# Optimization experiments

Hardware: AMD Instinct MI355X
Metric: run time of the kernel (lower is better)

Reference implementation:

```python
import jax, jax.numpy as jnp
import numpy as np

B, N, C, H = 2, 2048, 512, 8
D = C // H  # head dim = 64
SCALE = C ** -0.5  # module uses heads_channels**-0.5 (full inner dim, not per-head)


def setup_inputs() -> dict:
    key = jax.random.key(0)
    ks = jax.random.split(key, 9)
    return {
        "q": jax.random.normal(ks[0], (B, N, C), jnp.float32),
        "kv": jax.random.normal(ks[1], (B, N, C), jnp.float32),
        "pos_q": jax.random.normal(ks[2], (B, N, D), jnp.float32),
        "pos_k": jax.random.normal(ks[3], (B, N, D), jnp.float32),
        "Wq": jax.random.normal(ks[4], (C, C), jnp.float32) * (C ** -0.5),
        "Wk": jax.random.normal(ks[5], (C, C), jnp.float32) * (C ** -0.5),
        "Wv": jax.random.normal(ks[6], (C, C), jnp.float32) * (C ** -0.5),
        "Wo": jax.random.normal(ks[7], (C, C), jnp.float32) * (C ** -0.5),
        "bo": jnp.zeros((C,), jnp.float32),
    }


def reference(q, kv, pos_q, pos_k, Wq, Wk, Wv, Wo, bo):
    # projections: [b n c] @ [c c] -> [b n c]
    qp = q @ Wq
    kp = kv @ Wk
    vp = kv @ Wv
    # split heads: b n (h d) -> b h n d
    split = lambda t: t.reshape(B, N, H, D).transpose(0, 2, 1, 3)
    qh, kh, vh = split(qp), split(kp), split(vp)
    # additive positional bias, broadcast over heads: b n d -> b 1 n d
    qh = qh + pos_q[:, None, :, :]
    kh = kh + pos_k[:, None, :, :]
    sim = jnp.einsum("bhid,bhjd->bhij", qh, kh) * SCALE
    attn = jax.nn.softmax(sim, axis=-1)
    out = jnp.einsum("bhij,bhjd->bhid", attn, vh)
    # merge heads: b h n d -> b n (h d)
    out = out.transpose(0, 2, 1, 3).reshape(B, N, C)
    return out @ Wo + bo
```

## Files before the change

### kernel.cpp

```cpp
#include <hip/hip_runtime.h>
#include <hip/hip_bf16.h>
#include <stdint.h>
#include <math.h>

static constexpr int kB = 2, kN = 2048, kC = 512, kH = 8, kD = 64;
static constexpr float kScaleL2E =
    (float)(0.044194173824159216 * 1.4426950408889634);
static constexpr float kShift = 12.0f;
static constexpr int kSplit = 4;
static constexpr size_t kSegF = (size_t)kB * kN * kC;

typedef short bf16x8 __attribute__((ext_vector_type(8)));
typedef short bf16x4 __attribute__((ext_vector_type(4)));
typedef float f32x4  __attribute__((ext_vector_type(4)));

__device__ __forceinline__ float bf2f(unsigned short u) {
  union { unsigned int i; float f; } v; v.i = ((unsigned int)u) << 16; return v.f;
}
__device__ __forceinline__ unsigned short f2bf(float f) {
  union { float f; unsigned int i; } v; v.f = f;
  unsigned int x = v.i;
  return (unsigned short)((x + 0x7FFFu + ((x >> 16) & 1u)) >> 16);
}
__device__ __forceinline__ short f2bs(float f) { return (short)f2bf(f); }
__device__ __forceinline__ unsigned int pack2_t(float lo, float hi) {
  union { float f; unsigned int i; } a, b; a.f = lo; b.f = hi;
  return (b.i & 0xFFFF0000u) | (a.i >> 16);
}

__device__ __forceinline__ int vcol(int k) {
  return 32 * (k >> 5) + ((k >> 2) & 3) * 8 + ((k >> 4) & 1) * 4;
}

__global__ __launch_bounds__(256) void prep_kernel(
    const float* __restrict__ q, const float* __restrict__ kv,
    const float* __restrict__ Wq, const float* __restrict__ Wk,
    const float* __restrict__ Wv,
    unsigned short* __restrict__ qbf, unsigned short* __restrict__ kvbf,
    unsigned short* __restrict__ wT)
{
  const int t = threadIdx.x;
  if (blockIdx.z == 0) {
    const int gid = blockIdx.x * 256 + t;
    #pragma unroll
    for (int it = 0; it < 8; ++it) {
      int i4 = gid + it * 65536;
      float4 a = *(const float4*)(q + (size_t)i4 * 4);
      float4 b = *(const float4*)(kv + (size_t)i4 * 4);
      bf16x4 ab = {f2bs(a.x), f2bs(a.y), f2bs(a.z), f2bs(a.w)};
      bf16x4 bb = {f2bs(b.x), f2bs(b.y), f2bs(b.z), f2bs(b.w)};
      *(bf16x4*)(qbf + (size_t)i4 * 4) = ab;
      *(bf16x4*)(kvbf + (size_t)i4 * 4) = bb;
    }
  } else {
    if (blockIdx.x >= 192) return;
    const int wsel = blockIdx.x >> 6;
    const int tile = blockIdx.x & 63;
    const int tr = tile >> 3, tc = tile & 7;
    const float* W = (wsel == 0) ? Wq : (wsel == 1 ? Wk : Wv);
    unsigned short* out = wT + (size_t)wsel * kC * kC;

    __shared__ __align__(16) float Ts[64][68];
    #pragma unroll
    for (int it = 0; it < 4; ++it) {
      int e = t + it * 256;
      int r = e >> 4, c4 = (e & 15) * 4;
      *(float4*)&Ts[r][c4] =
          *(const float4*)(W + (size_t)(tr * 64 + r) * kC + tc * 64 + c4);
    }
    __syncthreads();
    const int n = t >> 2, ks = (t & 3) * 16;
    unsigned short* orow = out + (size_t)(tc * 64 + n) * kC + tr * 64 + ks;
    #pragma unroll
    for (int c = 0; c < 4; ++c) {
      ushort4 o;
      o.x = f2bf(Ts[ks + c * 4 + 0][n]);
      o.y = f2bf(Ts[ks + c * 4 + 1][n]);
      o.z = f2bf(Ts[ks + c * 4 + 2][n]);
      o.w = f2bf(Ts[ks + c * 4 + 3][n]);
      *(ushort4*)(orow + c * 4) = o;
    }
  }
}

__global__ __launch_bounds__(256) void proj_kernel(
    const unsigned short* __restrict__ qbf,
    const unsigned short* __restrict__ kvbf,
    const unsigned short* __restrict__ wT,
    const float* __restrict__ pos_q,
    const float* __restrict__ pos_k,
    unsigned short* __restrict__ qh,
    unsigned short* __restrict__ kh,
    unsigned short* __restrict__ vhT)
{
  const bool kvmode = (blockIdx.z == 1);
  const unsigned short* A = kvmode ? kvbf : qbf;
  const unsigned short* Bt0 = wT + (kvmode ? (size_t)kC * kC : 0);
  const unsigned short* Bt1 = wT + 2 * (size_t)kC * kC;

  __shared__ __align__(16) unsigned short As[128][72];
  __shared__ __align__(16) unsigned short Bs[2][64][72];

  const int t = threadIdx.x;
  const int w = t >> 6, lane = t & 63;
  const int l15 = lane & 15, quad = lane >> 4;
  const int m0 = blockIdx.x * 128;
  const int n0 = blockIdx.y * 64;

  const int sr = t >> 3, sc = (t & 7) * 8;

  bf16x8 pa[4], pb0[2], pb1[2];
  #pragma unroll
  for (int i = 0; i < 4; ++i)
    pa[i] = *(const bf16x8*)(A + (size_t)(m0 + sr + i * 32) * kC + sc);
  #pragma unroll
  for (int i = 0; i < 2; ++i)
    pb0[i] = *(const bf16x8*)(Bt0 + (size_t)(n0 + sr + i * 32) * kC + sc);
  if (kvmode)
    #pragma unroll
    for (int i = 0; i < 2; ++i)
      pb1[i] = *(const bf16x8*)(Bt1 + (size_t)(n0 + sr + i * 32) * kC + sc);

  f32x4 acc0[2][4], acc1[2][4];
  #pragma unroll
  for (int si = 0; si < 2; ++si)
    #pragma unroll
    for (int ct = 0; ct < 4; ++ct) {
      acc0[si][ct] = (f32x4){0.f, 0.f, 0.f, 0.f};
      acc1[si][ct] = (f32x4){0.f, 0.f, 0.f, 0.f};
    }

  for (int k0 = 0; k0 < kC; k0 += 64) {
    if (k0) __syncthreads();
    #pragma unroll
    for (int i = 0; i < 4; ++i) *(bf16x8*)&As[sr + i * 32][sc] = pa[i];
    #pragma unroll
    for (int i = 0; i < 2; ++i) *(bf16x8*)&Bs[0][sr + i * 32][sc] = pb0[i];
    if (kvmode)
      #pragma unroll
      for (int i = 0; i < 2; ++i) *(bf16x8*)&Bs[1][sr + i * 32][sc] = pb1[i];
    __syncthreads();
    if (k0 + 64 < kC) {
      int kn = k0 + 64;
      #pragma unroll
      for (int i = 0; i < 4; ++i)
        pa[i] = *(const bf16x8*)(A + (size_t)(m0 + sr + i * 32) * kC + kn + sc);
      #pragma unroll
      for (int i = 0; i < 2; ++i)
        pb0[i] = *(const bf16x8*)(Bt0 + (size_t)(n0 + sr + i * 32) * kC + kn + sc);
      if (kvmode)
        #pragma unroll
        for (int i = 0; i < 2; ++i)
          pb1[i] = *(const bf16x8*)(Bt1 + (size_t)(n0 + sr + i * 32) * kC + kn + sc);
    }
    bf16x8 a0[2], a1[2];
    #pragma unroll
    for (int si = 0; si < 2; ++si) {
      a0[si] = *(const bf16x8*)&As[w * 32 + si * 16 + l15][quad * 8];
      a1[si] = *(const bf16x8*)&As[w * 32 + si * 16 + l15][32 + quad * 8];
    }
    #pragma unroll
    for (int ct = 0; ct < 4; ++ct) {
      bf16x8 b0 = *(const bf16x8*)&Bs[0][ct * 16 + l15][quad * 8];
      bf16x8 b1 = *(const bf16x8*)&Bs[0][ct * 16 + l15][32 + quad * 8];
      #pragma unroll
      for (int si = 0; si < 2; ++si) {
        acc0[si][ct] = __builtin_amdgcn_mfma_f32_16x16x32_bf16(a0[si], b0, acc0[si][ct], 0, 0, 0);
        acc0[si][ct] = __builtin_amdgcn_mfma_f32_16x16x32_bf16(a1[si], b1, acc0[si][ct], 0, 0, 0);
      }
      if (kvmode) {
        bf16x8 c0 = *(const bf16x8*)&Bs[1][ct * 16 + l15][quad * 8];
        bf16x8 c1 = *(const bf16x8*)&Bs[1][ct * 16 + l15][32 + quad * 8];
        #pragma unroll
        for (int si = 0; si < 2; ++si) {
          acc1[si][ct] = __builtin_amdgcn_mfma_f32_16x16x32_bf16(a0[si], c0, acc1[si][ct], 0, 0, 0);
          acc1[si][ct] = __builtin_amdgcn_mfma_f32_16x16x32_bf16(a1[si], c1, acc1[si][ct], 0, 0, 0);
        }
      }
    }
  }

  const int h = n0 >> 6;
  if (!kvmode) {
    #pragma unroll
    for (int si = 0; si < 2; ++si)
      #pragma unroll
      for (int r = 0; r < 4; ++r) {
        int m = m0 + w * 32 + si * 16 + quad * 4 + r;
        int b = m >> 11, n_seq = m & (kN - 1);
        #pragma unroll
        for (int ct = 0; ct < 4; ++ct) {
          int d = ct * 16 + l15;
          float val = (acc0[si][ct][r] +
                       pos_q[((size_t)b * kN + n_seq) * kD + d]) * kScaleL2E;
          qh[(((size_t)b * kH + h) * kN + n_seq) * kD + d] = f2bf(val);
        }
      }
  } else {
    #pragma unroll
    for (int si = 0; si < 2; ++si)
      #pragma unroll
      for (int r = 0; r < 4; ++r) {
        int m = m0 + w * 32 + si * 16 + quad * 4 + r;
        int b = m >> 11, n_seq = m & (kN - 1);
        #pragma unroll
        for (int ct = 0; ct < 4; ++ct) {
          int d = ct * 16 + l15;
          float vk = acc0[si][ct][r] + pos_k[((size_t)b * kN + n_seq) * kD + d];
          kh[(((size_t)b * kH + h) * kN + n_seq) * kD + d] = f2bf(vk);
        }
      }
    __syncthreads();
    unsigned short (*Tv)[136] = (unsigned short(*)[136])&As[0][0];
    #pragma unroll
    for (int si = 0; si < 2; ++si)
      #pragma unroll
      for (int ct = 0; ct < 4; ++ct) {
        const int d = ct * 16 + l15;
        const int nl = w * 32 + si * 16 + quad * 4;
        unsigned int lo = (unsigned int)f2bf(acc1[si][ct][0]) |
                          ((unsigned int)f2bf(acc1[si][ct][1]) << 16);
        unsigned int hi = (unsigned int)f2bf(acc1[si][ct][2]) |
                          ((unsigned int)f2bf(acc1[si][ct][3]) << 16);
        *(unsigned int*)&Tv[d][nl]     = lo;
        *(unsigned int*)&Tv[d][nl + 2] = hi;
      }
    __syncthreads();
    const int c16 = t & 15, dr = t >> 4;
    const int b2 = m0 >> 11, nbase = m0 & (kN - 1);
    #pragma unroll
    for (int rep = 0; rep < 4; ++rep) {
      const int d = rep * 16 + dr;
      bf16x8 vv = *(const bf16x8*)&Tv[d][c16 * 8];
      *(bf16x8*)(vhT + (((size_t)(b2 * kH + h)) * kD + d) * kN + nbase + c16 * 8) = vv;
    }
  }
}

__global__ __launch_bounds__(256, 4) void attn_kernel(
    const unsigned short* __restrict__ qh,
    const unsigned short* __restrict__ kh,
    const unsigned short* __restrict__ vhT,
    unsigned short* __restrict__ opart,
    float* __restrict__ lbuf)
{
  const int bh = blockIdx.y;
  const int b = bh >> 3, h = bh & 7;
  const int q0 = blockIdx.x * 128;
  const int s = blockIdx.z;
  const int kbase = s * (kN / kSplit);
  const int nkt = kN / kSplit / 64;
  const int t = threadIdx.x;
  const int w = t >> 6, lane = t & 63;
  const int l15 = lane & 15, quad = lane >> 4;

  __shared__ __align__(16) unsigned short Kbf[2][64][72];
  __shared__ __align__(16) unsigned short Vt[2][64][72];

  const unsigned short* Qb = qh  + (size_t)bh * kN * kD;
  const unsigned short* Kb = kh  + (size_t)bh * kN * kD;
  const unsigned short* Vb = vhT + (size_t)bh * kD * kN;

  bf16x8 aq[2][2];
  #pragma unroll
  for (int g = 0; g < 2; ++g) {
    const unsigned short* qrow = Qb + (size_t)(q0 + w * 32 + g * 16 + l15) * kD;
    aq[g][0] = *(const bf16x8*)(qrow + quad * 8);
    aq[g][1] = *(const bf16x8*)(qrow + 32 + quad * 8);
  }

  const int sr = t >> 3, sc = (t & 7) * 8, sr2 = sr + 32;
  const int vc1 = vcol(sc), vc2 = vcol(sc + 4);

  bf16x8 pk0 = *(const bf16x8*)(Kb + (size_t)(kbase + sr) * kD + sc);
  bf16x8 pk1 = *(const bf16x8*)(Kb + (size_t)(kbase + sr2) * kD + sc);
  bf16x8 pv0 = *(const bf16x8*)(Vb + (size_t)sr * kN + kbase + sc);
  bf16x8 pv1 = *(const bf16x8*)(Vb + (size_t)sr2 * kN + kbase + sc);
  *(bf16x8*)&Kbf[0][sr][sc]  = pk0;
  *(bf16x8*)&Kbf[0][sr2][sc] = pk1;
  {
    bf16x4 lo0 = {pv0[0], pv0[1], pv0[2], pv0[3]};
    bf16x4 hi0 = {pv0[4], pv0[5], pv0[6], pv0[7]};
    bf16x4 lo1 = {pv1[0], pv1[1], pv1[2], pv1[3]};
    bf16x4 hi1 = {pv1[4], pv1[5], pv1[6], pv1[7]};
    *(bf16x4*)&Vt[0][sr][vc1]  = lo0;
    *(bf16x4*)&Vt[0][sr][vc2]  = hi0;
    *(bf16x4*)&Vt[0][sr2][vc1] = lo1;
    *(bf16x4*)&Vt[0][sr2][vc2] = hi1;
  }
  {
    int kt1 = kbase + 64;
    pk0 = *(const bf16x8*)(Kb + (size_t)(kt1 + sr) * kD + sc);
    pk1 = *(const bf16x8*)(Kb + (size_t)(kt1 + sr2) * kD + sc);
    pv0 = *(const bf16x8*)(Vb + (size_t)sr * kN + kt1 + sc);
    pv1 = *(const bf16x8*)(Vb + (size_t)sr2 * kN + kt1 + sc);
  }

  f32x4 o[2][4];
  #pragma unroll
  for (int g = 0; g < 2; ++g)
    #pragma unroll
    for (int nt = 0; nt < 4; ++nt) o[g][nt] = (f32x4){0.f, 0.f, 0.f, 0.f};
  float l_run[2] = {0.f, 0.f};

  for (int i = 0; i < nkt; ++i) {
    __syncthreads();
    if (i + 1 < nkt) {
      unsigned short (*Kw)[72] = Kbf[(i + 1) & 1];
      unsigned short (*Vw)[72] = Vt[(i + 1) & 1];
      *(bf16x8*)&Kw[sr][sc]  = pk0;
      *(bf16x8*)&Kw[sr2][sc] = pk1;
      bf16x4 lo0 = {pv0[0], pv0[1], pv0[2], pv0[3]};
      bf16x4 hi0 = {pv0[4], pv0[5], pv0[6], pv0[7]};
      bf16x4 lo1 = {pv1[0], pv1[1], pv1[2], pv1[3]};
      bf16x4 hi1 = {pv1[4], pv1[5], pv1[6], pv1[7]};
      *(bf16x4*)&Vw[sr][vc1]  = lo0;
      *(bf16x4*)&Vw[sr][vc2]  = hi0;
      *(bf16x4*)&Vw[sr2][vc1] = lo1;
      *(bf16x4*)&Vw[sr2][vc2] = hi1;
      if (i + 2 < nkt) {
        int ktn = kbase + (i + 2) * 64;
        pk0 = *(const bf16x8*)(Kb + (size_t)(ktn + sr) * kD + sc);
        pk1 = *(const bf16x8*)(Kb + (size_t)(ktn + sr2) * kD + sc);
        pv0 = *(const bf16x8*)(Vb + (size_t)sr * kN + ktn + sc);
        pv1 = *(const bf16x8*)(Vb + (size_t)sr2 * kN + ktn + sc);
      }
    }
    const unsigned short (*Kr)[72] = Kbf[i & 1];
    const unsigned short (*Vr)[72] = Vt[i & 1];

    f32x4 sacc[2][4];
    __builtin_amdgcn_s_setprio(1);
    #pragma unroll
    for (int ct = 0; ct < 4; ++ct) {
      bf16x8 ak0 = *(const bf16x8*)&Kr[ct * 16 + l15][quad * 8];
      bf16x8 ak1 = *(const bf16x8*)&Kr[ct * 16 + l15][32 + quad * 8];
      #pragma unroll
      for (int g = 0; g < 2; ++g) {
        f32x4 zz = (f32x4){0.f, 0.f, 0.f, 0.f};
        zz = __builtin_amdgcn_mfma_f32_16x16x32_bf16(ak0, aq[g][0], zz, 0, 0, 0);
        zz = __builtin_amdgcn_mfma_f32_16x16x32_bf16(ak1, aq[g][1], zz, 0, 0, 0);
        sacc[g][ct] = zz;
      }
    }
    __builtin_amdgcn_s_setprio(0);

    union PB8 { unsigned int u[4]; bf16x8 v; } pb01[2], pb23[2];
    #pragma unroll
    for (int g = 0; g < 2; ++g) {
      float psum = 0.f;
      #pragma unroll
      for (int ct = 0; ct < 4; ++ct)
        #pragma unroll
        for (int r = 0; r < 4; ++r) {
          float p = exp2f(sacc[g][ct][r] - kShift);
          sacc[g][ct][r] = p;
          psum += p;
        }
      l_run[g] += psum;
      pb01[g].u[0] = pack2_t(sacc[g][0][0], sacc[g][0][1]);
      pb01[g].u[1] = pack2_t(sacc[g][0][2], sacc[g][0][3]);
      pb01[g].u[2] = pack2_t(sacc[g][1][0], sacc[g][1][1]);
      pb01[g].u[3] = pack2_t(sacc[g][1][2], sacc[g][1][3]);
      pb23[g].u[0] = pack2_t(sacc[g][2][0], sacc[g][2][1]);
      pb23[g].u[1] = pack2_t(sacc[g][2][2], sacc[g][2][3]);
      pb23[g].u[2] = pack2_t(sacc[g][3][0], sacc[g][3][1]);
      pb23[g].u[3] = pack2_t(sacc[g][3][2], sacc[g][3][3]);
    }

    __builtin_amdgcn_s_setprio(1);
    #pragma unroll
    for (int nt = 0; nt < 4; ++nt) {
      bf16x8 av0 = *(const bf16x8*)&Vr[nt * 16 + l15][quad * 8];
      bf16x8 av1 = *(const bf16x8*)&Vr[nt * 16 + l15][32 + quad * 8];
      #pragma unroll
      for (int g = 0; g < 2; ++g) {
        o[g][nt] = __builtin_amdgcn_mfma_f32_16x16x32_bf16(av0, pb01[g].v, o[g][nt], 0, 0, 0);
        o[g][nt] = __builtin_amdgcn_mfma_f32_16x16x32_bf16(av1, pb23[g].v, o[g][nt], 0, 0, 0);
      }
    }
    __builtin_amdgcn_s_setprio(0);
  }

  #pragma unroll
  for (int g = 0; g < 2; ++g) {
    l_run[g] += __shfl_xor(l_run[g], 16);
    l_run[g] += __shfl_xor(l_run[g], 32);
  }
  if (quad == 0)
    #pragma unroll
    for (int g = 0; g < 2; ++g)
      lbuf[(size_t)(s * 16 + bh) * kN + q0 + w * 32 + g * 16 + l15] = l_run[g];

  __syncthreads();
  unsigned short (*Ot)[72] = (unsigned short(*)[72])&Kbf[0][0][0];
  #pragma unroll
  for (int g = 0; g < 2; ++g) {
    const int ql = w * 32 + g * 16 + l15;
    #pragma unroll
    for (int nt = 0; nt < 4; ++nt) {
      unsigned int lo = (unsigned int)f2bf(o[g][nt][0]) |
                        ((unsigned int)f2bf(o[g][nt][1]) << 16);
      unsigned int hi = (unsigned int)f2bf(o[g][nt][2]) |
                        ((unsigned int)f2bf(o[g][nt][3]) << 16);
      const int d0 = nt * 16 + quad * 4;
      *(unsigned int*)&Ot[ql][d0]     = lo;
      *(unsigned int*)&Ot[ql][d0 + 2] = hi;
    }
  }
  __syncthreads();
  {
    unsigned short* od = opart + (size_t)s * kSegF;
    const int c8 = t & 7, qb = t >> 3;
    #pragma unroll
    for (int rep = 0; rep < 4; ++rep) {
      const int ql = rep * 32 + qb;
      bf16x8 vv = *(const bf16x8*)&Ot[ql][c8 * 8];
      *(bf16x8*)(od + ((size_t)b * kN + (q0 + ql)) * kC + h * kD + c8 * 8) = vv;
    }
  }
}

__global__ __launch_bounds__(256) void proj_out_kernel(
    const unsigned short* __restrict__ opart,
    const float* __restrict__ lbuf,
    const float* __restrict__ Wo,
    const float* __restrict__ bo,
    float* __restrict__ out)
{
  __shared__ __align__(16) unsigned short Wt[64][72];

  const int t = threadIdx.x;
  const int w = t >> 6, lane = t & 63;
  const int l15 = lane & 15, quad = lane >> 4;
  const int m0 = blockIdx.x * 64;
  const int n0 = blockIdx.y * 64;

  const int m = m0 + w * 16 + l15;
  const int nseq = m & (kN - 1);
  const int bb = m >> 11;
  const size_t arow = (size_t)m * kC;

  ushort4 pw[4];
  #pragma unroll
  for (int i = 0; i < 4; ++i) {
    int e = t + i * 256;
    int r = e >> 4, c4 = (e & 15) * 4;
    float4 wv = *(const float4*)(Wo + (size_t)r * kC + n0 + c4);
    pw[i] = make_ushort4(f2bf(wv.x), f2bf(wv.y), f2bf(wv.z), f2bf(wv.w));
  }

  f32x4 acc[4];
  #pragma unroll
  for (int ct = 0; ct < 4; ++ct) acc[ct] = (f32x4){0.f, 0.f, 0.f, 0.f};

  #pragma unroll
  for (int k0 = 0; k0 < kC; k0 += 64) {
    if (k0) __syncthreads();
    #pragma unroll
    for (int i = 0; i < 4; ++i) {
      int e = t + i * 256;
      int r = e >> 4, c4 = (e & 15) * 4;
      Wt[c4 + 0][r] = pw[i].x;
      Wt[c4 + 1][r] = pw[i].y;
      Wt[c4 + 2][r] = pw[i].z;
      Wt[c4 + 3][r] = pw[i].w;
    }
    __syncthreads();

    const int h = k0 >> 6;
    const int bh = bb * 8 + h;
    float lsum = 0.f;
    #pragma unroll
    for (int s = 0; s < kSplit; ++s)
      lsum += lbuf[(size_t)(s * 16 + bh) * kN + nseq];
    const float wgt = 1.f / lsum;

    float af0[8] = {}, af1[8] = {};
    #pragma unroll
    for (int s = 0; s < kSplit; ++s) {
      bf16x8 v0 = *(const bf16x8*)(opart + (size_t)s * kSegF + arow + k0 + quad * 8);
      bf16x8 v1 = *(const bf16x8*)(opart + (size_t)s * kSegF + arow + k0 + 32 + quad * 8);
      #pragma unroll
      for (int j = 0; j < 8; ++j) {
        af0[j] += bf2f((unsigned short)v0[j]);
        af1[j] += bf2f((unsigned short)v1[j]);
      }
    }
    bf16x8 a0, a1;
    #pragma unroll
    for (int j = 0; j < 8; ++j) {
      a0[j] = (short)f2bf(af0[j] * wgt);
      a1[j] = (short)f2bf(af1[j] * wgt);
    }

    if (k0 + 64 < kC) {
      int kn = k0 + 64;
      #pragma unroll
      for (int i = 0; i < 4; ++i) {
        int e = t + i * 256;
        int r = e >> 4, c4 = (e & 15) * 4;
        float4 wv = *(const float4*)(Wo + (size_t)(kn + r) * kC + n0 + c4);
        pw[i] = make_ushort4(f2bf(wv.x), f2bf(wv.y), f2bf(wv.z), f2bf(wv.w));
      }
    }
    #pragma unroll
    for (int ct = 0; ct < 4; ++ct) {
      bf16x8 b0 = *(const bf16x8*)&Wt[ct * 16 + l15][quad * 8];
      bf16x8 b1 = *(const bf16x8*)&Wt[ct * 16 + l15][32 + quad * 8];
      acc[ct] = __builtin_amdgcn_mfma_f32_16x16x32_bf16(a0, b0, acc[ct], 0, 0, 0);
      acc[ct] = __builtin_amdgcn_mfma_f32_16x16x32_bf16(a1, b1, acc[ct], 0, 0, 0);
    }
  }

  #pragma unroll
  for (int ct = 0; ct < 4; ++ct) {
    int n = n0 + ct * 16 + l15;
    float bb2 = bo[n];
    #pragma unroll
    for (int r = 0; r < 4; ++r) {
      int mm = m0 + w * 16 + quad * 4 + r;
      out[(size_t)mm * kC + n] = acc[ct][r] + bb2;
    }
  }
}

extern "C" void kernel_launch(void* const* d_in, const int* in_sizes, int n_in,
                              void* d_out, int out_size, void* d_ws, size_t ws_size,
                              hipStream_t stream) {
  (void)in_sizes; (void)n_in; (void)out_size; (void)ws_size;
  const float* q     = (const float*)d_in[0];
  const float* kv    = (const float*)d_in[1];
  const float* pos_q = (const float*)d_in[2];
  const float* pos_k = (const float*)d_in[3];
  const float* Wq    = (const float*)d_in[4];
  const float* Wk    = (const float*)d_in[5];
  const float* Wv    = (const float*)d_in[6];
  const float* Wo    = (const float*)d_in[7];
  const float* bo    = (const float*)d_in[8];
  float* out = (float*)d_out;

  const size_t seg = (size_t)kB * kH * kN * kD;

  unsigned short* qbf  = (unsigned short*)d_ws;
  unsigned short* kvbf = qbf + seg;
  unsigned short* wT   = kvbf + seg;
  unsigned short* qhp  = wT + 3 * (size_t)kC * kC;
  unsigned short* khp  = qhp + seg;
  unsigned short* vtp  = khp + seg;
  unsigned short* opart = vtp + seg;
  float* lbuf = (float*)(opart + (size_t)kSplit * kSegF);

  dim3 blk(256);
  prep_kernel<<<dim3(256, 1, 2), blk, 0, stream>>>(q, kv, Wq, Wk, Wv, qbf, kvbf, wT);
  proj_kernel<<<dim3(32, 8, 2), blk, 0, stream>>>(qbf, kvbf, wT, pos_q, pos_k,
                                                  qhp, khp, vtp);
  attn_kernel<<<dim3(16, 16, kSplit), blk, 0, stream>>>(qhp, khp, vtp, opart, lbuf);
  proj_out_kernel<<<dim3(64, 8), blk, 0, stream>>>(opart, lbuf, Wo, bo, out);
}
```

Before: 161.6 us.

## Halve attention query tile, single-buffer K/V, remap blocks with XCD-aware swizzle

The attention kernel now gives each block 64 query rows instead of 128, one 16-row group per wave. K/V use a single LDS buffer with an extra barrier per tile instead of double buffering, and the next tile's K and V global loads are spread across the loop body. The grid is flattened to 2048 blocks with a swizzled index so consecutive blocks land on the same split/head, and launch bounds target 8 blocks per CU. The aim is higher occupancy and L2 locality, at the cost of reloading K/V twice as often per query and an additional synchronization per iteration.

```diff
diff --git a/kernel.cpp b/kernel.cpp
--- a/kernel.cpp
+++ b/kernel.cpp
@@ -237,36 +237,36 @@
   }
 }
 
-__global__ __launch_bounds__(256, 4) void attn_kernel(
+__global__ __launch_bounds__(256, 8) void attn_kernel(
     const unsigned short* __restrict__ qh,
     const unsigned short* __restrict__ kh,
     const unsigned short* __restrict__ vhT,
     unsigned short* __restrict__ opart,
     float* __restrict__ lbuf)
 {
-  const int bh = blockIdx.y;
+  const int sid = (blockIdx.x & 7) * 256 + (blockIdx.x >> 3);
+  const int s  = sid >> 9;
+  const int bh = (sid >> 5) & 15;
+  const int q0 = (sid & 31) * 64;
   const int b = bh >> 3, h = bh & 7;
-  const int q0 = blockIdx.x * 128;
-  const int s = blockIdx.z;
   const int kbase = s * (kN / kSplit);
   const int nkt = kN / kSplit / 64;
   const int t = threadIdx.x;
   const int w = t >> 6, lane = t & 63;
   const int l15 = lane & 15, quad = lane >> 4;
 
-  __shared__ __align__(16) unsigned short Kbf[2][64][72];
-  __shared__ __align__(16) unsigned short Vt[2][64][72];
+  __shared__ __align__(16) unsigned short Kb_s[64][72];
+  __shared__ __align__(16) unsigned short Vt_s[64][72];
 
   const unsigned short* Qb = qh  + (size_t)bh * kN * kD;
   const unsigned short* Kb = kh  + (size_t)bh * kN * kD;
   const unsigned short* Vb = vhT + (size_t)bh * kD * kN;
 
-  bf16x8 aq[2][2];
-  #pragma unroll
-  for (int g = 0; g < 2; ++g) {
-    const unsigned short* qrow = Qb + (size_t)(q0 + w * 32 + g * 16 + l15) * kD;
-    aq[g][0] = *(const bf16x8*)(qrow + quad * 8);
-    aq[g][1] = *(const bf16x8*)(qrow + 32 + quad * 8);
+  bf16x8 aq0, aq1;
+  {
+    const unsigned short* qrow = Qb + (size_t)(q0 + w * 16 + l15) * kD;
+    aq0 = *(const bf16x8*)(qrow + quad * 8);
+    aq1 = *(const bf16x8*)(qrow + 32 + quad * 8);
   }
 
   const int sr = t >> 3, sc = (t & 7) * 8, sr2 = sr + 32;
@@ -276,133 +276,101 @@
   bf16x8 pk1 = *(const bf16x8*)(Kb + (size_t)(kbase + sr2) * kD + sc);
   bf16x8 pv0 = *(const bf16x8*)(Vb + (size_t)sr * kN + kbase + sc);
   bf16x8 pv1 = *(const bf16x8*)(Vb + (size_t)sr2 * kN + kbase + sc);
-  *(bf16x8*)&Kbf[0][sr][sc]  = pk0;
-  *(bf16x8*)&Kbf[0][sr2][sc] = pk1;
-  {
-    bf16x4 lo0 = {pv0[0], pv0[1], pv0[2], pv0[3]};
-    bf16x4 hi0 = {pv0[4], pv0[5], pv0[6], pv0[7]};
-    bf16x4 lo1 = {pv1[0], pv1[1], pv1[2], pv1[3]};
-    bf16x4 hi1 = {pv1[4], pv1[5], pv1[6], pv1[7]};
-    *(bf16x4*)&Vt[0][sr][vc1]  = lo0;
-    *(bf16x4*)&Vt[0][sr][vc2]  = hi0;
-    *(bf16x4*)&Vt[0][sr2][vc1] = lo1;
-    *(bf16x4*)&Vt[0][sr2][vc2] = hi1;
-  }
-  {
-    int kt1 = kbase + 64;
-    pk0 = *(const bf16x8*)(Kb + (size_t)(kt1 + sr) * kD + sc);
-    pk1 = *(const bf16x8*)(Kb + (size_t)(kt1 + sr2) * kD + sc);
-    pv0 = *(const bf16x8*)(Vb + (size_t)sr * kN + kt1 + sc);
-    pv1 = *(const bf16x8*)(Vb + (size_t)sr2 * kN + kt1 + sc);
-  }
-
-  f32x4 o[2][4];
-  #pragma unroll
-  for (int g = 0; g < 2; ++g)
-    #pragma unroll
-    for (int nt = 0; nt < 4; ++nt) o[g][nt] = (f32x4){0.f, 0.f, 0.f, 0.f};
-  float l_run[2] = {0.f, 0.f};
+
+  f32x4 o[4];
+  #pragma unroll
+  for (int nt = 0; nt < 4; ++nt) o[nt] = (f32x4){0.f, 0.f, 0.f, 0.f};
+  float l_run = 0.f;
 
   for (int i = 0; i < nkt; ++i) {
     __syncthreads();
-    if (i + 1 < nkt) {
-      unsigned short (*Kw)[72] = Kbf[(i + 1) & 1];
-      unsigned short (*Vw)[72] = Vt[(i + 1) & 1];
-      *(bf16x8*)&Kw[sr][sc]  = pk0;
-      *(bf16x8*)&Kw[sr2][sc] = pk1;
+    *(bf16x8*)&Kb_s[sr][sc]  = pk0;
+    *(bf16x8*)&Kb_s[sr2][sc] = pk1;
+    {
       bf16x4 lo0 = {pv0[0], pv0[1], pv0[2], pv0[3]};
       bf16x4 hi0 = {pv0[4], pv0[5], pv0[6], pv0[7]};
       bf16x4 lo1 = {pv1[0], pv1[1], pv1[2], pv1[3]};
       bf16x4 hi1 = {pv1[4], pv1[5], pv1[6], pv1[7]};
-      *(bf16x4*)&Vw[sr][vc1]  = lo0;
-      *(bf16x4*)&Vw[sr][vc2]  = hi0;
-      *(bf16x4*)&Vw[sr2][vc1] = lo1;
-      *(bf16x4*)&Vw[sr2][vc2] = hi1;
-      if (i + 2 < nkt) {
-        int ktn = kbase + (i + 2) * 64;
-        pk0 = *(const bf16x8*)(Kb + (size_t)(ktn + sr) * kD + sc);
-        pk1 = *(const bf16x8*)(Kb + (size_t)(ktn + sr2) * kD + sc);
-        pv0 = *(const bf16x8*)(Vb + (size_t)sr * kN + ktn + sc);
-        pv1 = *(const bf16x8*)(Vb + (size_t)sr2 * kN + ktn + sc);
-      }
-    }
-    const unsigned short (*Kr)[72] = Kbf[i & 1];
-    const unsigned short (*Vr)[72] = Vt[i & 1];
-
-    f32x4 sacc[2][4];
+      *(bf16x4*)&Vt_s[sr][vc1]  = lo0;
+      *(bf16x4*)&Vt_s[sr][vc2]  = hi0;
+      *(bf16x4*)&Vt_s[sr2][vc1] = lo1;
+      *(bf16x4*)&Vt_s[sr2][vc2] = hi1;
+    }
+    __syncthreads();
+
+    f32x4 sacc[4];
     __builtin_amdgcn_s_setprio(1);
     #pragma unroll
     for (int ct = 0; ct < 4; ++ct) {
-      bf16x8 ak0 = *(const bf16x8*)&Kr[ct * 16 + l15][quad * 8];
-      bf16x8 ak1 = *(const bf16x8*)&Kr[ct * 16 + l15][32 + quad * 8];
-      #pragma unroll
-      for (int g = 0; g < 2; ++g) {
-        f32x4 zz = (f32x4){0.f, 0.f, 0.f, 0.f};
-        zz = __builtin_amdgcn_mfma_f32_16x16x32_bf16(ak0, aq[g][0], zz, 0, 0, 0);
-        zz = __builtin_amdgcn_mfma_f32_16x16x32_bf16(ak1, aq[g][1], zz, 0, 0, 0);
-        sacc[g][ct] = zz;
-      }
+      bf16x8 ak0 = *(const bf16x8*)&Kb_s[ct * 16 + l15][quad * 8];
+      bf16x8 ak1 = *(const bf16x8*)&Kb_s[ct * 16 + l15][32 + quad * 8];
+      f32x4 zz = (f32x4){0.f, 0.f, 0.f, 0.f};
+      zz = __builtin_amdgcn_mfma_f32_16x16x32_bf16(ak0, aq0, zz, 0, 0, 0);
+      zz = __builtin_amdgcn_mfma_f32_16x16x32_bf16(ak1, aq1, zz, 0, 0, 0);
+      sacc[ct] = zz;
     }
     __builtin_amdgcn_s_setprio(0);
 
-    union PB8 { unsigned int u[4]; bf16x8 v; } pb01[2], pb23[2];
-    #pragma unroll
-    for (int g = 0; g < 2; ++g) {
+    if (i + 1 < nkt) {
+      int ktn = kbase + (i + 1) * 64;
+      pk0 = *(const bf16x8*)(Kb + (size_t)(ktn + sr) * kD + sc);
+      pk1 = *(const bf16x8*)(Kb + (size_t)(ktn + sr2) * kD + sc);
+    }
+
+    union PB8 { unsigned int u[4]; bf16x8 v; } pb01, pb23;
+    {
       float psum = 0.f;
       #pragma unroll
       for (int ct = 0; ct < 4; ++ct)
         #pragma unroll
         for (int r = 0; r < 4; ++r) {
-          float p = exp2f(sacc[g][ct][r] - kShift);
-          sacc[g][ct][r] = p;
+          float p = exp2f(sacc[ct][r] - kShift);
+          sacc[ct][r] = p;
           psum += p;
         }
-      l_run[g] += psum;
-      pb01[g].u[0] = pack2_t(sacc[g][0][0], sacc[g][0][1]);
-      pb01[g].u[1] = pack2_t(sacc[g][0][2], sacc[g][0][3]);
-      pb01[g].u[2] = pack2_t(sacc[g][1][0], sacc[g][1][1]);
-      pb01[g].u[3] = pack2_t(sacc[g][1][2], sacc[g][1][3]);
-      pb23[g].u[0] = pack2_t(sacc[g][2][0], sacc[g][2][1]);
-      pb23[g].u[1] = pack2_t(sacc[g][2][2], sacc[g][2][3]);
-      pb23[g].u[2] = pack2_t(sacc[g][3][0], sacc[g][3][1]);
-      pb23[g].u[3] = pack2_t(sacc[g][3][2], sacc[g][3][3]);
+      l_run += psum;
+      pb01.u[0] = pack2_t(sacc[0][0], sacc[0][1]);
+      pb01.u[1] = pack2_t(sacc[0][2], sacc[0][3]);
+      pb01.u[2] = pack2_t(sacc[1][0], sacc[1][1]);
+      pb01.u[3] = pack2_t(sacc[1][2], sacc[1][3]);
+      pb23.u[0] = pack2_t(sacc[2][0], sacc[2][1]);
+      pb23.u[1] = pack2_t(sacc[2][2], sacc[2][3]);
+      pb23.u[2] = pack2_t(sacc[3][0], sacc[3][1]);
+      pb23.u[3] = pack2_t(sacc[3][2], sacc[3][3]);
+    }
+
+    if (i + 1 < nkt) {
+      int ktn = kbase + (i + 1) * 64;
+      pv0 = *(const bf16x8*)(Vb + (size_t)sr * kN + ktn + sc);
+      pv1 = *(const bf16x8*)(Vb + (size_t)sr2 * kN + ktn + sc);
     }
 
     __builtin_amdgcn_s_setprio(1);
     #pragma unroll
     for (int nt = 0; nt < 4; ++nt) {
-      bf16x8 av0 = *(const bf16x8*)&Vr[nt * 16 + l15][quad * 8];
-      bf16x8 av1 = *(const bf16x8*)&Vr[nt * 16 + l15][32 + quad * 8];
-      #pragma unroll
-      for (int g = 0; g < 2; ++g) {
-        o[g][nt] = __builtin_amdgcn_mfma_f32_16x16x32_bf16(av0, pb01[g].v, o[g][nt], 0, 0, 0);
-        o[g][nt] = __builtin_amdgcn_mfma_f32_16x16x32_bf16(av1, pb23[g].v, o[g][nt], 0, 0, 0);
-      }
+      bf16x8 av0 = *(const bf16x8*)&Vt_s[nt * 16 + l15][quad * 8];
+      bf16x8 av1 = *(const bf16x8*)&Vt_s[nt * 16 + l15][32 + quad * 8];
+      o[nt] = __builtin_amdgcn_mfma_f32_16x16x32_bf16(av0, pb01.v, o[nt], 0, 0, 0);
+      o[nt] = __builtin_amdgcn_mfma_f32_16x16x32_bf16(av1, pb23.v, o[nt], 0, 0, 0);
     }
     __builtin_amdgcn_s_setprio(0);
   }
 
-  #pragma unroll
-  for (int g = 0; g < 2; ++g) {
-    l_run[g] += __shfl_xor(l_run[g], 16);
-    l_run[g] += __shfl_xor(l_run[g], 32);
-  }
+  l_run += __shfl_xor(l_run, 16);
+  l_run += __shfl_xor(l_run, 32);
   if (quad == 0)
-    #pragma unroll
-    for (int g = 0; g < 2; ++g)
-      lbuf[(size_t)(s * 16 + bh) * kN + q0 + w * 32 + g * 16 + l15] = l_run[g];
+    lbuf[(size_t)(s * 16 + bh) * kN + q0 + w * 16 + l15] = l_run;
 
   __syncthreads();
-  unsigned short (*Ot)[72] = (unsigned short(*)[72])&Kbf[0][0][0];
-  #pragma unroll
-  for (int g = 0; g < 2; ++g) {
-    const int ql = w * 32 + g * 16 + l15;
+  unsigned short (*Ot)[72] = (unsigned short(*)[72])&Kb_s[0][0];
+  {
+    const int ql = w * 16 + l15;
     #pragma unroll
     for (int nt = 0; nt < 4; ++nt) {
-      unsigned int lo = (unsigned int)f2bf(o[g][nt][0]) |
-                        ((unsigned int)f2bf(o[g][nt][1]) << 16);
-      unsigned int hi = (unsigned int)f2bf(o[g][nt][2]) |
-                        ((unsigned int)f2bf(o[g][nt][3]) << 16);
+      unsigned int lo = (unsigned int)f2bf(o[nt][0]) |
+                        ((unsigned int)f2bf(o[nt][1]) << 16);
+      unsigned int hi = (unsigned int)f2bf(o[nt][2]) |
+                        ((unsigned int)f2bf(o[nt][3]) << 16);
       const int d0 = nt * 16 + quad * 4;
       *(unsigned int*)&Ot[ql][d0]     = lo;
       *(unsigned int*)&Ot[ql][d0 + 2] = hi;
@@ -413,7 +381,7 @@
     unsigned short* od = opart + (size_t)s * kSegF;
     const int c8 = t & 7, qb = t >> 3;
     #pragma unroll
-    for (int rep = 0; rep < 4; ++rep) {
+    for (int rep = 0; rep < 2; ++rep) {
       const int ql = rep * 32 + qb;
       bf16x8 vv = *(const bf16x8*)&Ot[ql][c8 * 8];
       *(bf16x8*)(od + ((size_t)b * kN + (q0 + ql)) * kC + h * kD + c8 * 8) = vv;
@@ -555,6 +523,6 @@
   prep_kernel<<<dim3(256, 1, 2), blk, 0, stream>>>(q, kv, Wq, Wk, Wv, qbf, kvbf, wT);
   proj_kernel<<<dim3(32, 8, 2), blk, 0, stream>>>(qbf, kvbf, wT, pos_q, pos_k,
                                                   qhp, khp, vtp);
-  attn_kernel<<<dim3(16, 16, kSplit), blk, 0, stream>>>(qhp, khp, vtp, opart, lbuf);
+  attn_kernel<<<dim3(2048), blk, 0, stream>>>(qhp, khp, vtp, opart, lbuf);
   proj_out_kernel<<<dim3(64, 8), blk, 0, stream>>>(opart, lbuf, Wo, bo, out);
 }
```

New measurement: 160.8 us. Within noise of the previous version (-0.5%).
